# Kernel tuning notes

Hardware: AMD Instinct MI355X
Metric: run time of the kernel (lower is better)

## Reference

```python
import jax, jax.numpy as jnp
import numpy as np

B, T = 64, 4096
H, I, F = 256, 7, 5
# MLP pyramid: in=H+F=261 -> 2^8..2^3 -> itera_dim
DIMS = [H + F, 256, 128, 64, 32, 16, 8, I]


def _uniform(key, shape, fan_in):
    s = 1.0 / np.sqrt(fan_in)
    return jax.random.uniform(key, shape, jnp.float32, -s, s)


def setup_inputs() -> dict:
    key = jax.random.key(0)
    ks = jax.random.split(key, 32)
    inp = {"x": jax.random.normal(ks[0], (B, T, I + F), jnp.float32)}
    # RNN params (torch nn.RNN layout: W_ih [H,I], W_hh [H,H])
    inp["W_ih"] = _uniform(ks[1], (H, I), H)
    inp["W_hh"] = _uniform(ks[2], (H, H), H)
    inp["b_ih"] = _uniform(ks[3], (H,), H)
    inp["b_hh"] = _uniform(ks[4], (H,), H)
    # fc_V linears
    for j, (din, dout) in enumerate(zip(DIMS[:-1], DIMS[1:])):
        inp[f"W{j}"] = _uniform(ks[5 + 2 * j], (dout, din), din)
        inp[f"b{j}"] = _uniform(ks[6 + 2 * j], (dout,), din)
    return inp


def reference(x, W_ih, W_hh, b_ih, b_hh,
              W0, b0, W1, b1, W2, b2, W3, b3, W4, b4, W5, b5, W6, b6):
    x_itera = x[..., :I]          # [B,T,I]
    x_fixed = x[..., I:]          # [B,T,F]
    # precompute input projection for the whole sequence (one big GEMM)
    xW = jnp.einsum('bti,hi->bth', x_itera, W_ih) + b_ih + b_hh  # [B,T,H]

    def step(h, xw_t):
        h = jnp.tanh(xw_t + h @ W_hh.T)
        return h, h

    h0 = jnp.zeros((x.shape[0], H), x.dtype)
    h_last, ht = jax.lax.scan(step, h0, jnp.swapaxes(xW, 0, 1))  # ht: [T,B,H]
    ht = jnp.swapaxes(ht, 0, 1)                                  # [B,T,H]

    z = jnp.concatenate([ht, x_fixed], axis=-1)                  # [B,T,H+F]
    for W, b in ((W0, b0), (W1, b1), (W2, b2), (W3, b3), (W4, b4), (W5, b5)):
        z = jax.nn.leaky_relu(z @ W.T + b, 0.01)
    ot = z @ W6.T + b6                                           # [B,T,I]
    return ot, h_last[None]                                      # ht_last: [1,B,H]
```

## Files before the change

### kernel.cpp

```cpp
#include <hip/hip_runtime.h>

#define BB 64
#define TT 4096
#define HH 256
#define NTOK (BB * TT)

typedef _Float16 f16;
typedef _Float16 f16x2 __attribute__((ext_vector_type(2)));
typedef _Float16 f16x8 __attribute__((ext_vector_type(8)));
typedef float f32x4 __attribute__((ext_vector_type(4)));
typedef unsigned int uint;
typedef unsigned short ushort;
typedef uint uint4v __attribute__((ext_vector_type(4)));

__device__ __forceinline__ uint packf16(float a, float b) {
    ushort lo = __builtin_bit_cast(ushort, (f16)a);
    ushort hi = __builtin_bit_cast(ushort, (f16)b);
    return (uint)lo | ((uint)hi << 16);
}

__global__ __launch_bounds__(256) void rnn_wswz_kernel(const float* __restrict__ Whh,
                                                       uint4v* __restrict__ Wsw) {
    int gid = blockIdx.x * 256 + threadIdx.x;
    if (gid >= 8192) return;
    int tid = gid >> 4, fi = gid & 15;
    int mt = fi >> 3, ks = fi & 7;
    int lane = tid & 63, w = tid >> 6;
    int hd = w * 32 + mt * 16 + (lane & 15);
    int kb = ks * 32 + ((lane >> 4) << 3);
    const float* p = Whh + hd * 256 + kb;
    uint4v v;
    v.x = packf16(p[0], p[1]);
    v.y = packf16(p[2], p[3]);
    v.z = packf16(p[4], p[5]);
    v.w = packf16(p[6], p[7]);
    Wsw[gid] = v;
}

__global__ __launch_bounds__(256) void bfrag_prep_kernel(const float* __restrict__ W,
                                                         uint4v* __restrict__ dst,
                                                         int N, int Kreal, int KS, int NT) {
    int gid = blockIdx.x * 256 + threadIdx.x;
    if (gid >= NT * KS * 64) return;
    int lane = gid & 63;
    int t = gid >> 6;
    int ks = t % KS, nt = t / KS;
    int n = nt * 16 + (lane & 15);
    int kb = ks * 32 + (lane >> 4) * 8;
    float f[8];
#pragma unroll
    for (int j = 0; j < 8; ++j) {
        int k = kb + j;
        f[j] = (n < N && k < Kreal) ? W[n * Kreal + k] : 0.f;
    }
    uint4v v;
    v.x = packf16(f[0], f[1]);
    v.y = packf16(f[2], f[3]);
    v.z = packf16(f[4], f[5]);
    v.w = packf16(f[6], f[7]);
    dst[gid] = v;
}

__global__ __launch_bounds__(512) __attribute__((amdgpu_waves_per_eu(2, 2))) void rnn_kernel(
        const float* __restrict__ x, const uint4v* __restrict__ Wsw,
        const float* __restrict__ Wih, const float* __restrict__ bih,
        const float* __restrict__ bhh, f16* __restrict__ ht, float* __restrict__ hlast) {
    const int b = blockIdx.x, tid = threadIdx.x;
    const int lane = tid & 63, w = tid >> 6;
    const int q = lane >> 4, bl = lane & 15;
    const int d = w * 32 + ((bl >> 3) << 4) + (q << 2) + (bl & 3);
    const bool writer = (bl & 4) == 0;
    __shared__ __align__(16) f16 hbuf[2][256];
    __shared__ uint4 xs[2][128];

    uint4v wv[16];
    {
        const uint4v* wp = Wsw + (size_t)tid * 16;
#pragma unroll
        for (int i = 0; i < 16; ++i) wv[i] = wp[i];
    }
#pragma unroll
    for (int i = 0; i < 16; ++i) asm volatile("" : "+v"(wv[i]));

    float wih[7];
#pragma unroll
    for (int i = 0; i < 7; ++i) wih[i] = Wih[d * 7 + i];
    const float bias = bih[d] + bhh[d];

    const float* xb = x + (size_t)b * TT * 12;
    uint4 xpre = make_uint4(0, 0, 0, 0);
    if (tid < 128) {
        int row = tid >> 1, u = tid & 1;
        xs[0][row * 2 + u] = *(const uint4*)(xb + row * 12 + u * 4);
        xpre = *(const uint4*)(xb + (64 + row) * 12 + u * 4);
        ((uint*)hbuf[0])[tid] = 0;
    }
    __syncthreads();

    f16* htp = ht + (size_t)b * TT * 256 + d;
    ushort hst[16];

    for (int tb = 0; tb < 256; ++tb) {
#pragma unroll
        for (int k = 0; k < 16; ++k) {
            const int t = tb * 16 + k;
            const int cur = k & 1;
            const int tile = (t >> 6) & 1, tstep = t & 63;

            const uint4v* hq = (const uint4v*)hbuf[cur];
            uint4v hfr[8];
#pragma unroll
            for (int ks = 0; ks < 8; ++ks) hfr[ks] = hq[ks * 4 + q];

            f32x4 a0 = (f32x4){0.f, 0.f, 0.f, 0.f}, a1 = a0, a2 = a0, a3 = a0;
#pragma unroll
            for (int kk = 0; kk < 4; ++kk) {
                f16x8 hlo = __builtin_bit_cast(f16x8, hfr[kk]);
                f16x8 hhi = __builtin_bit_cast(f16x8, hfr[4 + kk]);
                a0 = __builtin_amdgcn_mfma_f32_16x16x32_f16(
                    __builtin_bit_cast(f16x8, wv[kk]), hlo, a0, 0, 0, 0);
                a1 = __builtin_amdgcn_mfma_f32_16x16x32_f16(
                    __builtin_bit_cast(f16x8, wv[4 + kk]), hhi, a1, 0, 0, 0);
                a2 = __builtin_amdgcn_mfma_f32_16x16x32_f16(
                    __builtin_bit_cast(f16x8, wv[8 + kk]), hlo, a2, 0, 0, 0);
                a3 = __builtin_amdgcn_mfma_f32_16x16x32_f16(
                    __builtin_bit_cast(f16x8, wv[12 + kk]), hhi, a3, 0, 0, 0);
            }

            const float4 xa = ((const float4*)xs[tile])[tstep * 2];
            const float4 xc = ((const float4*)xs[tile])[tstep * 2 + 1];
            float xw = fmaf(xa.x, wih[0], bias);
            xw = fmaf(xa.y, wih[1], xw);
            xw = fmaf(xa.z, wih[2], xw);
            xw = fmaf(xa.w, wih[3], xw);
            xw = fmaf(xc.x, wih[4], xw);
            xw = fmaf(xc.y, wih[5], xw);
            xw = fmaf(xc.z, wih[6], xw);

            f32x4 acc0 = a0 + a1;
            f32x4 acc1 = a2 + a3;

            float s0 = (bl & 8) ? acc1[0] : acc0[0];
            float s1 = (bl & 8) ? acc1[1] : acc0[1];
            float s2 = (bl & 8) ? acc1[2] : acc0[2];
            float s3 = (bl & 8) ? acc1[3] : acc0[3];
            float p01 = (bl & 1) ? s1 : s0;
            float p23 = (bl & 1) ? s3 : s2;
            float pre = ((bl & 2) ? p23 : p01) + xw;

            float e = __builtin_amdgcn_exp2f(-2.885390082f * pre);
            float rr = __builtin_amdgcn_rcpf(1.0f + e);
            float h = fmaf(2.0f, rr, -1.0f);

            f16 hf = (f16)h;
            if (writer) hbuf[cur ^ 1][d] = hf;
            hst[k] = __builtin_bit_cast(ushort, hf);
            if (tb == 255 && k == 15 && writer) hlast[b * 256 + d] = h;

            if (tstep == 32 && tid < 128) {
                int row = tid >> 1, u = tid & 1;
                xs[tile ^ 1][row * 2 + u] = xpre;
                int nt = (t & ~63) + 128 + row;
                if (nt > TT - 1) nt = TT - 1;
                xpre = *(const uint4*)(xb + nt * 12 + u * 4);
            }
            asm volatile("s_waitcnt lgkmcnt(0)\n\ts_barrier" ::: "memory");
        }
        if (writer) {
            const size_t base = (size_t)(tb * 16) * 256;
#pragma unroll
            for (int k = 0; k < 16; ++k)
                htp[base + (size_t)k * 256] = __builtin_bit_cast(f16, hst[k]);
        }
    }
}

struct MlpB {
    const uint4v* bf[7];
    const float* bias[7];
};

template <int KS, int NT, bool MSPLIT>
__device__ __forceinline__ void mfma_layer(const uint4v* __restrict__ Bf,
                                           const float* __restrict__ bias, int Nreal,
                                           const uint4v* zin, uint4v* zout,
                                           int w, int lane, int m15, int q) {
    constexpr int NW = MSPLIT ? NT : (NT / 4);
    constexpr int MW = MSPLIT ? 1 : 4;
    const int ntb = MSPLIT ? 0 : w * NW;
    const int mtb = MSPLIT ? w : 0;
    f32x4 acc[MW][NW];
#pragma unroll
    for (int i = 0; i < MW; ++i)
#pragma unroll
        for (int j = 0; j < NW; ++j) acc[i][j] = (f32x4){0.f, 0.f, 0.f, 0.f};

#pragma unroll
    for (int ks = 0; ks < KS; ++ks) {
        f16x8 a[MW];
#pragma unroll
        for (int mt = 0; mt < MW; ++mt)
            a[mt] = __builtin_bit_cast(f16x8, zin[((mtb + mt) * 16 + m15) * 37 + ks * 4 + q]);
#pragma unroll
        for (int nt = 0; nt < NW; ++nt) {
            f16x8 b = __builtin_bit_cast(f16x8, Bf[((size_t)(ntb + nt) * KS + ks) * 64 + lane]);
#pragma unroll
            for (int mt = 0; mt < MW; ++mt)
                acc[mt][nt] =
                    __builtin_amdgcn_mfma_f32_16x16x32_f16(a[mt], b, acc[mt][nt], 0, 0, 0);
        }
    }
    f16* zo = (f16*)zout;
#pragma unroll
    for (int nt = 0; nt < NW; ++nt) {
        const int col = (ntb + nt) * 16 + m15;
        const float bv = (col < Nreal) ? bias[col] : 0.f;
#pragma unroll
        for (int mt = 0; mt < MW; ++mt) {
#pragma unroll
            for (int r = 0; r < 4; ++r) {
                float v = acc[mt][nt][r] + bv;
                v = fmaxf(v, 0.01f * v);
                const int row = (mtb + mt) * 16 + q * 4 + r;
                zo[row * 296 + col] = (f16)v;
            }
        }
    }
}

__global__ __launch_bounds__(256) void mlp_kernel(const f16* __restrict__ ht,
                                                  const float* __restrict__ x,
                                                  MlpB P, float* __restrict__ out) {
    __shared__ uint4v z0[64 * 37];
    __shared__ uint4v z1[64 * 37];
    const int tid = threadIdx.x;
    const int w = tid >> 6, lane = tid & 63;
    const int m15 = lane & 15, q = lane >> 4;
    const int tok0 = blockIdx.x * 64;

    for (int i = tid; i < 64 * 32; i += 256) {
        int r = i >> 5, u = i & 31;
        z0[r * 37 + u] = ((const uint4v*)(ht + (size_t)(tok0 + r) * 256))[u];
    }
    for (int i = tid; i < 64 * 5; i += 256) {
        int r = i / 5, u = 32 + (i % 5);
        uint4v v = {0u, 0u, 0u, 0u};
        if (u == 32) {
            const float* xp = x + (size_t)(tok0 + r) * 12 + 7;
            v.x = packf16(xp[0], xp[1]);
            v.y = packf16(xp[2], xp[3]);
            v.z = packf16(xp[4], 0.f);
        }
        z0[r * 37 + u] = v;
    }
    __syncthreads();

    mfma_layer<9, 16, false>(P.bf[0], P.bias[0], 256, z0, z1, w, lane, m15, q);
    __syncthreads();
    mfma_layer<8, 8, false>(P.bf[1], P.bias[1], 128, z1, z0, w, lane, m15, q);
    __syncthreads();
    mfma_layer<4, 4, false>(P.bf[2], P.bias[2], 64, z0, z1, w, lane, m15, q);
    __syncthreads();
    mfma_layer<2, 2, true>(P.bf[3], P.bias[3], 32, z1, z0, w, lane, m15, q);
    __syncthreads();
    mfma_layer<1, 1, true>(P.bf[4], P.bias[4], 16, z0, z1, w, lane, m15, q);
    __syncthreads();
    mfma_layer<1, 1, true>(P.bf[5], P.bias[5], 8, z1, z0, w, lane, m15, q);
    __syncthreads();

    {
        f16x8 a = __builtin_bit_cast(f16x8, z0[(w * 16 + m15) * 37 + q]);
        f16x8 b = __builtin_bit_cast(f16x8, P.bf[6][lane]);
        f32x4 acc = (f32x4){0.f, 0.f, 0.f, 0.f};
        acc = __builtin_amdgcn_mfma_f32_16x16x32_f16(a, b, acc, 0, 0, 0);
        if (m15 < 7) {
            const float bv = P.bias[6][m15];
#pragma unroll
            for (int r = 0; r < 4; ++r)
                out[(size_t)(tok0 + w * 16 + q * 4 + r) * 7 + m15] = acc[r] + bv;
        }
    }
}

extern "C" void kernel_launch(void* const* d_in, const int* in_sizes, int n_in,
                              void* d_out, int out_size, void* d_ws, size_t ws_size,
                              hipStream_t stream) {
    const float* x = (const float*)d_in[0];
    const float* Wih = (const float*)d_in[1];
    const float* Whh = (const float*)d_in[2];
    const float* bih = (const float*)d_in[3];
    const float* bhh = (const float*)d_in[4];
    const float* W[7];
    const float* bb[7];
    for (int j = 0; j < 7; ++j) {
        W[j] = (const float*)d_in[5 + 2 * j];
        bb[j] = (const float*)d_in[6 + 2 * j];
    }
    float* out = (float*)d_out;

    static const int Kd[7] = {261, 256, 128, 64, 32, 16, 8};
    static const int Nd[7] = {256, 128, 64, 32, 16, 8, 7};
    static const int KSd[7] = {9, 8, 4, 2, 1, 1, 1};
    static const int NTd[7] = {16, 8, 4, 2, 1, 1, 1};

    char* ws = (char*)d_ws;
    f16* ht = (f16*)ws;
    size_t off = (size_t)NTOK * HH * 2;
    uint4v* Wsw = (uint4v*)(ws + off);
    off += (size_t)8192 * 16;
    uint4v* bfp[7];
    for (int j = 0; j < 7; ++j) {
        bfp[j] = (uint4v*)(ws + off);
        off += (size_t)NTd[j] * KSd[j] * 64 * 16;
    }

    rnn_wswz_kernel<<<32, 256, 0, stream>>>(Whh, Wsw);
    for (int j = 0; j < 7; ++j) {
        int cnt = NTd[j] * KSd[j] * 64;
        bfrag_prep_kernel<<<(cnt + 255) / 256, 256, 0, stream>>>(W[j], bfp[j], Nd[j], Kd[j],
                                                                 KSd[j], NTd[j]);
    }

    rnn_kernel<<<BB, 512, 0, stream>>>(x, Wsw, Wih, bih, bhh, ht, out + (size_t)NTOK * 7);

    MlpB P;
    for (int j = 0; j < 7; ++j) {
        P.bf[j] = bfp[j];
        P.bias[j] = bb[j];
    }
    mlp_kernel<<<NTOK / 64, 256, 0, stream>>>(ht, x, P, out);
}
```

Before: 1.900 ms.

## Precompute input projection in a separate kernel and prefetch it in RNN loop

```diff
diff --git a/kernel.cpp b/kernel.cpp
--- a/kernel.cpp
+++ b/kernel.cpp
@@ -6,7 +6,6 @@
 #define NTOK (BB * TT)
 
 typedef _Float16 f16;
-typedef _Float16 f16x2 __attribute__((ext_vector_type(2)));
 typedef _Float16 f16x8 __attribute__((ext_vector_type(8)));
 typedef float f32x4 __attribute__((ext_vector_type(4)));
 typedef unsigned int uint;
@@ -37,6 +36,32 @@
     Wsw[gid] = v;
 }
 
+__global__ __launch_bounds__(256) void xw_prep_kernel(const float* __restrict__ x,
+                                                      const float* __restrict__ Wih,
+                                                      const float* __restrict__ bih,
+                                                      const float* __restrict__ bhh,
+                                                      float* __restrict__ xwp) {
+    int gid = blockIdx.x * 256 + threadIdx.x;
+    int token = gid >> 6;
+    if (token >= NTOK) return;
+    int dq = (gid & 63) << 2;
+    const float* xp = x + (size_t)token * 12;
+    float xv[7];
+#pragma unroll
+    for (int i = 0; i < 7; ++i) xv[i] = xp[i];
+    float4 o;
+    float* op = &o.x;
+#pragma unroll
+    for (int j = 0; j < 4; ++j) {
+        int dd = dq + j;
+        float xw = fmaf(xv[0], Wih[dd * 7 + 0], bih[dd] + bhh[dd]);
+#pragma unroll
+        for (int i = 1; i < 7; ++i) xw = fmaf(xv[i], Wih[dd * 7 + i], xw);
+        op[j] = xw;
+    }
+    *(float4*)(xwp + (size_t)token * 256 + dq) = o;
+}
+
 __global__ __launch_bounds__(256) void bfrag_prep_kernel(const float* __restrict__ W,
                                                          uint4v* __restrict__ dst,
                                                          int N, int Kreal, int KS, int NT) {
@@ -62,6 +87,97 @@
 }
 
 __global__ __launch_bounds__(512) __attribute__((amdgpu_waves_per_eu(2, 2))) void rnn_kernel(
+        const float* __restrict__ xwp, const uint4v* __restrict__ Wsw,
+        f16* __restrict__ ht, float* __restrict__ hlast) {
+    const int b = blockIdx.x, tid = threadIdx.x;
+    const int lane = tid & 63, w = tid >> 6;
+    const int q = lane >> 4, bl = lane & 15;
+    const int d = w * 32 + ((bl >> 3) << 4) + (q << 2) + (bl & 3);
+    const bool writer = (bl & 4) == 0;
+    __shared__ __align__(16) f16 hbuf[2][256];
+
+    uint4v wv[16];
+    {
+        const uint4v* wp = Wsw + (size_t)tid * 16;
+#pragma unroll
+        for (int i = 0; i < 16; ++i) wv[i] = wp[i];
+    }
+#pragma unroll
+    for (int i = 0; i < 16; ++i) asm volatile("" : "+v"(wv[i]));
+
+    if (tid < 128) ((uint*)hbuf[0])[tid] = 0;
+    __syncthreads();
+
+    f16* htp = ht + (size_t)b * TT * 256 + d;
+    const float* xg = xwp + (size_t)b * TT * 256 + d;
+    float xwA = xg[0];
+    float xwB = xg[256];
+    ushort hst[16];
+
+    for (int tb = 0; tb < 256; ++tb) {
+#pragma unroll
+        for (int k = 0; k < 16; ++k) {
+            const int t = tb * 16 + k;
+            const int cur = k & 1;
+
+            const uint4v* hq = (const uint4v*)hbuf[cur];
+            uint4v hfr[8];
+#pragma unroll
+            for (int ks = 0; ks < 8; ++ks) hfr[ks] = hq[ks * 4 + q];
+
+            f32x4 a0 = (f32x4){0.f, 0.f, 0.f, 0.f}, a1 = a0, a2 = a0, a3 = a0;
+#pragma unroll
+            for (int kk = 0; kk < 4; ++kk) {
+                f16x8 hlo = __builtin_bit_cast(f16x8, hfr[kk]);
+                f16x8 hhi = __builtin_bit_cast(f16x8, hfr[4 + kk]);
+                a0 = __builtin_amdgcn_mfma_f32_16x16x32_f16(
+                    __builtin_bit_cast(f16x8, wv[kk]), hlo, a0, 0, 0, 0);
+                a1 = __builtin_amdgcn_mfma_f32_16x16x32_f16(
+                    __builtin_bit_cast(f16x8, wv[4 + kk]), hhi, a1, 0, 0, 0);
+                a2 = __builtin_amdgcn_mfma_f32_16x16x32_f16(
+                    __builtin_bit_cast(f16x8, wv[8 + kk]), hlo, a2, 0, 0, 0);
+                a3 = __builtin_amdgcn_mfma_f32_16x16x32_f16(
+                    __builtin_bit_cast(f16x8, wv[12 + kk]), hhi, a3, 0, 0, 0);
+            }
+
+            int tn = t + 2;
+            if (tn > TT - 1) tn = TT - 1;
+            float xwN = xg[(size_t)tn * 256];
+
+            f32x4 acc0 = a0 + a1;
+            f32x4 acc1 = a2 + a3;
+
+            float s0 = (bl & 8) ? acc1[0] : acc0[0];
+            float s1 = (bl & 8) ? acc1[1] : acc0[1];
+            float s2 = (bl & 8) ? acc1[2] : acc0[2];
+            float s3 = (bl & 8) ? acc1[3] : acc0[3];
+            float p01 = (bl & 1) ? s1 : s0;
+            float p23 = (bl & 1) ? s3 : s2;
+            float pre = ((bl & 2) ? p23 : p01) + xwA;
+
+            float e = __builtin_amdgcn_exp2f(-2.885390082f * pre);
+            float rr = __builtin_amdgcn_rcpf(1.0f + e);
+            float h = fmaf(2.0f, rr, -1.0f);
+
+            f16 hf = (f16)h;
+            if (writer) hbuf[cur ^ 1][d] = hf;
+            hst[k] = __builtin_bit_cast(ushort, hf);
+            if (tb == 255 && k == 15 && writer) hlast[b * 256 + d] = h;
+
+            xwA = xwB;
+            xwB = xwN;
+            asm volatile("s_waitcnt lgkmcnt(0)\n\ts_barrier" ::: "memory");
+        }
+        if (writer) {
+            const size_t base = (size_t)(tb * 16) * 256;
+#pragma unroll
+            for (int k = 0; k < 16; ++k)
+                htp[base + (size_t)k * 256] = __builtin_bit_cast(f16, hst[k]);
+        }
+    }
+}
+
+__global__ __launch_bounds__(512) __attribute__((amdgpu_waves_per_eu(2, 2))) void rnn_fb_kernel(
         const float* __restrict__ x, const uint4v* __restrict__ Wsw,
         const float* __restrict__ Wih, const float* __restrict__ bih,
         const float* __restrict__ bhh, f16* __restrict__ ht, float* __restrict__ hlast) {
@@ -313,6 +429,9 @@
         bfp[j] = (uint4v*)(ws + off);
         off += (size_t)NTd[j] * KSd[j] * 64 * 16;
     }
+    size_t xw_bytes = (size_t)NTOK * HH * 4;
+    bool use_xw = (ws_size >= off + xw_bytes);
+    float* xwp = (float*)(ws + off);
 
     rnn_wswz_kernel<<<32, 256, 0, stream>>>(Whh, Wsw);
     for (int j = 0; j < 7; ++j) {
@@ -321,7 +440,13 @@
                                                                  KSd[j], NTd[j]);
     }
 
-    rnn_kernel<<<BB, 512, 0, stream>>>(x, Wsw, Wih, bih, bhh, ht, out + (size_t)NTOK * 7);
+    if (use_xw) {
+        xw_prep_kernel<<<NTOK / 4, 256, 0, stream>>>(x, Wih, bih, bhh, xwp);
+        rnn_kernel<<<BB, 512, 0, stream>>>(xwp, Wsw, ht, out + (size_t)NTOK * 7);
+    } else {
+        rnn_fb_kernel<<<BB, 512, 0, stream>>>(x, Wsw, Wih, bih, bhh, ht,
+                                              out + (size_t)NTOK * 7);
+    }
 
     MlpB P;
     for (int j = 0; j < 7; ++j) {
```

Measured after the change: 1.891 ms. No clear change (-0.5%).
